# Kernel tuning notes

Hardware: AMD Instinct MI355X
Metric: run time of the kernel (lower is better)

The kernel has to match this reference:

```python
import jax, jax.numpy as jnp
import numpy as np

# irreps: node = 64x0e + 32x1o (dim 160), edge = 1x0e + 1x1o (dim 4)
N, E = 50000, 800000
MUL0, MUL1 = 64, 32
D = MUL0 + 3 * MUL1  # 160
INV3 = float(1.0 / np.sqrt(3.0))   # w3j(0,1,1) / w3j(1,1,0) component
INV6 = float(1.0 / np.sqrt(6.0))   # w3j(1,1,1) component (eps/sqrt(6))
C0 = float(1.0 / np.sqrt(MUL0 + MUL1))          # sqrt(dim_out=1 / fan_in=96) for 0e output
C1 = float(np.sqrt(3.0 / (MUL0 + 2 * MUL1)))    # sqrt(dim_out=3 / fan_in=128) for 1o output
LIN_S = float(1.0 / np.sqrt(MUL0))
LIN_V = float(1.0 / np.sqrt(MUL1))


def setup_inputs() -> dict:
    key = jax.random.key(0)
    ks = jax.random.split(key, 10)
    x = jax.random.normal(ks[0], (N, D), dtype=jnp.float32)
    sh = jax.random.normal(ks[1], (E, 4), dtype=jnp.float32)
    edge_index = jax.random.randint(ks[2], (2, E), 0, N, dtype=jnp.int64)
    # FullyConnectedTensorProduct path weights (mul2 = 1 squeezed out)
    W1 = jax.random.normal(ks[3], (MUL0, MUL0), dtype=jnp.float32)  # 0e x 0e -> 0e
    W2 = jax.random.normal(ks[4], (MUL1, MUL0), dtype=jnp.float32)  # 1o x 1o -> 0e
    W3 = jax.random.normal(ks[5], (MUL0, MUL1), dtype=jnp.float32)  # 0e x 1o -> 1o
    W4 = jax.random.normal(ks[6], (MUL1, MUL1), dtype=jnp.float32)  # 1o x 0e -> 1o
    W5 = jax.random.normal(ks[7], (MUL1, MUL1), dtype=jnp.float32)  # 1o x 1o -> 1o
    # equivariant Linear (block-diagonal per irrep type)
    Ws = jax.random.normal(ks[8], (MUL0, MUL0), dtype=jnp.float32)
    Wv = jax.random.normal(ks[9], (MUL1, MUL1), dtype=jnp.float32)
    return {"x": x, "sh": sh, "W1": W1, "W2": W2, "W3": W3, "W4": W4,
            "W5": W5, "Ws": Ws, "Wv": Wv, "edge_index": edge_index}


def reference(x, sh, W1, W2, W3, W4, W5, Ws, Wv, edge_index):
    n = x.shape[0]
    src, dst = edge_index[0], edge_index[1]
    s = x[:, :MUL0]                              # (N, 64)   0e
    v = x[:, MUL0:].reshape(n, MUL1, 3)          # (N, 32, 3) 1o
    ss, vv = s[src], v[src]                      # gather: (E,64), (E,32,3)
    e0 = sh[:, 0:1]                              # (E,1)
    e1 = sh[:, 1:4]                              # (E,3)

    # --- CG tensor product per edge ---
    # 0e output
    dot = jnp.einsum('eui,ei->eu', vv, e1)       # 1o x 1o -> 0e
    out0 = C0 * ((ss * e0) @ W1 + (dot * INV3) @ W2)          # (E,64)
    # 1o output
    p3 = (ss @ W3)[:, :, None] * e1[:, None, :] * INV3         # 0e x 1o -> 1o
    p4 = jnp.einsum('eui,uw->ewi', vv * e0[:, :, None], W4) * INV3  # 1o x 0e -> 1o
    p5 = jnp.einsum('eui,uw->ewi', jnp.cross(vv, e1[:, None, :]), W5) * INV6  # 1o x 1o -> 1o
    out1 = C1 * (p3 + p4 + p5)                   # (E,32,3)

    m = jnp.concatenate([out0, out1.reshape(-1, 3 * MUL1)], axis=1)  # (E,160)
    m_agg = jax.ops.segment_sum(m, dst, num_segments=n)              # scatter-add

    # --- equivariant Linear (block per irrep) ---
    hs = (m_agg[:, :MUL0] @ Ws) * LIN_S
    hv = jnp.einsum('nui,uw->nwi', m_agg[:, MUL0:].reshape(n, MUL1, 3), Wv) * LIN_V
    h = jnp.concatenate([hs, hv.reshape(n, 3 * MUL1)], axis=1)
    return x + jax.nn.relu(h)
```

## Files before the change

### kernel.cpp

```cpp
#include <hip/hip_runtime.h>

#define DFEAT 160

typedef float  f4v __attribute__((ext_vector_type(4)));
typedef short  s8v __attribute__((ext_vector_type(8)));

__device__ __constant__ float kINV3 = 0.57735026918962576451f;
__device__ __constant__ float kINV6 = 0.40824829046386301637f;
__device__ __constant__ float kC0   = 0.10206207261596575f;
__device__ __constant__ float kC1   = 0.15309310892394863f;
__device__ __constant__ float kLS   = 0.125f;
__device__ __constant__ float kLV   = 0.17677669529663687f;

#define WAVE_SYNC() do { \
    asm volatile("s_waitcnt lgkmcnt(0)" ::: "memory"); \
    __builtin_amdgcn_sched_barrier(0); \
} while (0)

#define MFMA(a, b, c) __builtin_amdgcn_mfma_f32_16x16x32_bf16((a), (b), (c), 0, 0, 0)

__device__ __forceinline__ unsigned f2bf(float f) {
    const unsigned u = __builtin_bit_cast(unsigned, f);
    const unsigned r = 0x7fffu + ((u >> 16) & 1u);
    return (u + r) >> 16;
}
__device__ __forceinline__ float bf2f(unsigned short u) {
    return __builtin_bit_cast(float, ((unsigned)u) << 16);
}

__global__ void hist_kernel(const int* __restrict__ dst, int* __restrict__ deg, int E) {
    for (int e = blockIdx.x * blockDim.x + threadIdx.x; e < E; e += gridDim.x * blockDim.x)
        atomicAdd(&deg[dst[e]], 1);
}

__global__ __launch_bounds__(256) void blocksum_kernel(const int* __restrict__ deg,
                                                       int* __restrict__ bsum, int N) {
    __shared__ int red[256];
    const int b = blockIdx.x, t = threadIdx.x;
    const int base = b * 1024;
    int s = 0;
    for (int i = t; i < 1024; i += 256) {
        const int idx = base + i;
        if (idx < N) s += (deg[idx] + 3) & ~3;
    }
    red[t] = s;
    __syncthreads();
    for (int off = 128; off > 0; off >>= 1) {
        if (t < off) red[t] += red[t + off];
        __syncthreads();
    }
    if (t == 0) bsum[b] = red[0];
}

__global__ void scanb_kernel(int* __restrict__ bsum, int nb, int* __restrict__ rowptrN) {
    if (threadIdx.x == 0 && blockIdx.x == 0) {
        int run = 0;
        for (int i = 0; i < nb; ++i) { const int v = bsum[i]; bsum[i] = run; run += v; }
        *rowptrN = run;
    }
}

__global__ __launch_bounds__(256) void scanfinal_kernel(const int* __restrict__ deg,
                                                        const int* __restrict__ bsum,
                                                        int* __restrict__ rowptr,
                                                        int* __restrict__ cursor,
                                                        int* __restrict__ src_sorted,
                                                        float4* __restrict__ sh_sorted,
                                                        int N) {
    __shared__ int ts[256];
    const int b = blockIdx.x, t = threadIdx.x;
    const int i0 = b * 1024 + t * 4;
    int dO[4], dP[4];
    #pragma unroll
    for (int j = 0; j < 4; ++j) {
        dO[j] = (i0 + j < N) ? deg[i0 + j] : 0;
        dP[j] = (dO[j] + 3) & ~3;
    }
    ts[t] = dP[0] + dP[1] + dP[2] + dP[3];
    __syncthreads();
    for (int off = 1; off < 256; off <<= 1) {
        const int v = (t >= off) ? ts[t - off] : 0;
        __syncthreads();
        ts[t] += v;
        __syncthreads();
    }
    int ex = bsum[b] + ((t == 0) ? 0 : ts[t - 1]);
    const float4 z4 = make_float4(0.f, 0.f, 0.f, 0.f);
    #pragma unroll
    for (int j = 0; j < 4; ++j) {
        if (i0 + j < N) {
            rowptr[i0 + j] = ex;
            cursor[i0 + j] = ex;
            for (int f = ex + dO[j]; f < ex + dP[j]; ++f) {
                src_sorted[f] = 0;
                sh_sorted[f] = z4;
            }
            ex += dP[j];
        }
    }
}

__global__ void scatter_kernel(const int* __restrict__ src, const int* __restrict__ dst,
                               const float4* __restrict__ sh, int* __restrict__ cursor,
                               int* __restrict__ src_sorted, float4* __restrict__ sh_sorted,
                               int E) {
    for (int e = blockIdx.x * blockDim.x + threadIdx.x; e < E; e += gridDim.x * blockDim.x) {
        const int pos = atomicAdd(&cursor[dst[e]], 1);
        src_sorted[pos] = src[e];
        sh_sorted[pos] = sh[e];
    }
}

__global__ __launch_bounds__(256) void prep_kernel(
    const float* __restrict__ x, int N,
    const float* __restrict__ W1, const float* __restrict__ W2,
    const float* __restrict__ W3, const float* __restrict__ W4,
    const float* __restrict__ W5, const float* __restrict__ Ws,
    const float* __restrict__ Wv,
    unsigned short* __restrict__ wtB, unsigned short* __restrict__ xq)
{
    const int total = 160 * 480 + N * 20;
    for (int i = blockIdx.x * 256 + threadIdx.x; i < total; i += gridDim.x * 256) {
        if (i < 160 * 480) {
            const int o = i;
            const int f = o / 480, k = o % 480;
            float v = 0.f;
            if (f < 64) {
                if (k < 64) {
                    float a = 0.f;
                    for (int m = 0; m < 64; ++m) a += W1[k * 64 + m] * Ws[m * 64 + f];
                    v = kLS * kC0 * a;
                } else if (k >= 256 && k < 288) {
                    float a = 0.f;
                    for (int m = 0; m < 64; ++m) a += W2[(k - 256) * 64 + m] * Ws[m * 64 + f];
                    v = kLS * kC0 * a;
                }
            } else {
                const int w = (f - 64) / 3, ii = (f - 64) % 3;
                if (k >= 64 + 64 * ii && k < 128 + 64 * ii) {
                    float a = 0.f;
                    const int kk = k - 64 - 64 * ii;
                    for (int m = 0; m < 32; ++m) a += W3[kk * 32 + m] * Wv[m * 32 + w];
                    v = kLV * kC1 * a;
                } else if (k >= 288 + 32 * ii && k < 320 + 32 * ii) {
                    float a = 0.f;
                    const int kk = k - 288 - 32 * ii;
                    for (int m = 0; m < 32; ++m) a += W4[kk * 32 + m] * Wv[m * 32 + w];
                    v = kLV * kC1 * a;
                } else if (k >= 384 + 32 * ii && k < 416 + 32 * ii) {
                    float a = 0.f;
                    const int kk = k - 384 - 32 * ii;
                    for (int m = 0; m < 32; ++m) a += W5[kk * 32 + m] * Wv[m * 32 + w];
                    v = kLV * kC1 * a;
                }
            }
            wtB[o] = (unsigned short)f2bf(v);
        } else {
            const int s = i - 160 * 480;
            const float4 a = ((const float4*)x)[2 * s + 0];
            const float4 b = ((const float4*)x)[2 * s + 1];
            int4 o;
            o.x = (int)(f2bf(a.x) | (f2bf(a.y) << 16));
            o.y = (int)(f2bf(a.z) | (f2bf(a.w) << 16));
            o.z = (int)(f2bf(b.x) | (f2bf(b.y) << 16));
            o.w = (int)(f2bf(b.z) | (f2bf(b.w) << 16));
            ((int4*)xq)[s] = o;
        }
    }
}

__global__ __launch_bounds__(256, 8) void agg_bf16_kernel(
    const unsigned short* __restrict__ xq, const float4* __restrict__ shs,
    const int* __restrict__ srcs, const int* __restrict__ rowptr,
    unsigned short* __restrict__ st_all, int N)
{
    const int tid  = threadIdx.x;
    const int lane = tid & 63;
    const int wid  = tid >> 6;
    const bool lo  = (lane < 32);
    const int  w   = lane & 31;

    for (int n = blockIdx.x * 4 + wid; n < N; n += gridDim.x * 4) {
        const int beg = rowptr[n];
        const int end = rowptr[n + 1];

        float r0 = 0.f, r1 = 0.f, r2 = 0.f, r3 = 0.f;
        float a2 = 0.f, a4x = 0.f, a4y = 0.f, a4z = 0.f;
        float a5x = 0.f, a5y = 0.f, a5z = 0.f;

#define PAIR(SA, SB, SHA, SHB) do { \
            const unsigned short* xa = xq + (size_t)(SA) * DFEAT; \
            const unsigned short* xb = xq + (size_t)(SB) * DFEAT; \
            const float xsA = bf2f(xa[lane]); \
            const float xsB = bf2f(xb[lane]); \
            const unsigned short* xh = lo ? xa : xb; \
            const float va = bf2f(xh[64 + 3 * w]); \
            const float vb = bf2f(xh[65 + 3 * w]); \
            const float vc = bf2f(xh[66 + 3 * w]); \
            r0 += (SHA).x * xsA;  r0 += (SHB).x * xsB; \
            r1 += (SHA).y * xsA;  r1 += (SHB).y * xsB; \
            r2 += (SHA).z * xsA;  r2 += (SHB).z * xsB; \
            r3 += (SHA).w * xsA;  r3 += (SHB).w * xsB; \
            const float he0  = lo ? (SHA).x : (SHB).x; \
            const float he1x = lo ? (SHA).y : (SHB).y; \
            const float he1y = lo ? (SHA).z : (SHB).z; \
            const float he1z = lo ? (SHA).w : (SHB).w; \
            a2  += va * he1x + vb * he1y + vc * he1z; \
            a4x += he0 * va;  a4y += he0 * vb;  a4z += he0 * vc; \
            a5x += vb * he1z;  a5x -= vc * he1y; \
            a5y += vc * he1x;  a5y -= va * he1z; \
            a5z += va * he1y;  a5z -= vb * he1x; \
        } while (0)

        for (int idx = beg; idx < end; idx += 4) {
            const int4 s4 = *(const int4*)(srcs + idx);
            const float4 shA = shs[idx + 0];
            const float4 shB = shs[idx + 1];
            const float4 shC = shs[idx + 2];
            const float4 shD = shs[idx + 3];
            PAIR(s4.x, s4.y, shA, shB);
            PAIR(s4.z, s4.w, shC, shD);
        }
#undef PAIR

        a2  += __shfl_xor(a2, 32);
        a4x += __shfl_xor(a4x, 32);
        a4y += __shfl_xor(a4y, 32);
        a4z += __shfl_xor(a4z, 32);
        a5x += __shfl_xor(a5x, 32);
        a5y += __shfl_xor(a5y, 32);
        a5z += __shfl_xor(a5z, 32);

        unsigned short* sr = st_all + (size_t)n * 480;
        sr[lane]       = (unsigned short)f2bf(r0);
        sr[64 + lane]  = (unsigned short)f2bf(kINV3 * r1);
        sr[128 + lane] = (unsigned short)f2bf(kINV3 * r2);
        sr[192 + lane] = (unsigned short)f2bf(kINV3 * r3);
        sr[256 + lane] = (unsigned short)f2bf(kINV3 * (lo ? a2 : a4x));
        sr[320 + lane] = (unsigned short)f2bf(lo ? (kINV3 * a4y) : (kINV3 * a4z));
        sr[384 + lane] = (unsigned short)f2bf(lo ? (kINV6 * a5x) : (kINV6 * a5y));
        if (lo) sr[448 + lane] = (unsigned short)f2bf(kINV6 * a5z);
    }
}

__global__ __launch_bounds__(256, 8) void agg_f32_kernel(
    const float* __restrict__ x, const float4* __restrict__ shs,
    const int* __restrict__ srcs, const int* __restrict__ rowptr,
    unsigned short* __restrict__ st_all, int N)
{
    const int tid  = threadIdx.x;
    const int lane = tid & 63;
    const int wid  = tid >> 6;
    const bool lo  = (lane < 32);
    const int  w   = lane & 31;

    for (int n = blockIdx.x * 4 + wid; n < N; n += gridDim.x * 4) {
        const int beg = rowptr[n];
        const int end = rowptr[n + 1];

        float r0 = 0.f, r1 = 0.f, r2 = 0.f, r3 = 0.f;
        float a2 = 0.f, a4x = 0.f, a4y = 0.f, a4z = 0.f;
        float a5x = 0.f, a5y = 0.f, a5z = 0.f;

#define PAIR(SA, SB, SHA, SHB) do { \
            const float* xa = x + (size_t)(SA) * DFEAT; \
            const float* xb = x + (size_t)(SB) * DFEAT; \
            const float xsA = xa[lane]; \
            const float xsB = xb[lane]; \
            const float* xh = lo ? xa : xb; \
            const float va = xh[64 + 3 * w]; \
            const float vb = xh[65 + 3 * w]; \
            const float vc = xh[66 + 3 * w]; \
            r0 += (SHA).x * xsA;  r0 += (SHB).x * xsB; \
            r1 += (SHA).y * xsA;  r1 += (SHB).y * xsB; \
            r2 += (SHA).z * xsA;  r2 += (SHB).z * xsB; \
            r3 += (SHA).w * xsA;  r3 += (SHB).w * xsB; \
            const float he0  = lo ? (SHA).x : (SHB).x; \
            const float he1x = lo ? (SHA).y : (SHB).y; \
            const float he1y = lo ? (SHA).z : (SHB).z; \
            const float he1z = lo ? (SHA).w : (SHB).w; \
            a2  += va * he1x + vb * he1y + vc * he1z; \
            a4x += he0 * va;  a4y += he0 * vb;  a4z += he0 * vc; \
            a5x += vb * he1z;  a5x -= vc * he1y; \
            a5y += vc * he1x;  a5y -= va * he1z; \
            a5z += va * he1y;  a5z -= vb * he1x; \
        } while (0)

        for (int idx = beg; idx < end; idx += 4) {
            const int4 s4 = *(const int4*)(srcs + idx);
            const float4 shA = shs[idx + 0];
            const float4 shB = shs[idx + 1];
            const float4 shC = shs[idx + 2];
            const float4 shD = shs[idx + 3];
            PAIR(s4.x, s4.y, shA, shB);
            PAIR(s4.z, s4.w, shC, shD);
        }
#undef PAIR

        a2  += __shfl_xor(a2, 32);
        a4x += __shfl_xor(a4x, 32);
        a4y += __shfl_xor(a4y, 32);
        a4z += __shfl_xor(a4z, 32);
        a5x += __shfl_xor(a5x, 32);
        a5y += __shfl_xor(a5y, 32);
        a5z += __shfl_xor(a5z, 32);

        unsigned short* sr = st_all + (size_t)n * 480;
        sr[lane]       = (unsigned short)f2bf(r0);
        sr[64 + lane]  = (unsigned short)f2bf(kINV3 * r1);
        sr[128 + lane] = (unsigned short)f2bf(kINV3 * r2);
        sr[192 + lane] = (unsigned short)f2bf(kINV3 * r3);
        sr[256 + lane] = (unsigned short)f2bf(kINV3 * (lo ? a2 : a4x));
        sr[320 + lane] = (unsigned short)f2bf(lo ? (kINV3 * a4y) : (kINV3 * a4z));
        sr[384 + lane] = (unsigned short)f2bf(lo ? (kINV6 * a5x) : (kINV6 * a5y));
        if (lo) sr[448 + lane] = (unsigned short)f2bf(kINV6 * a5z);
    }
}

__global__ __launch_bounds__(256, 4) void transform_kernel(
    const float* __restrict__ x, const unsigned short* __restrict__ st_all,
    const unsigned short* __restrict__ wtB, float* __restrict__ out, int N)
{
    __shared__ float sEp[4][16][17];
    const int tid  = threadIdx.x;
    const int lane = tid & 63;
    const int wid  = tid >> 6;
    const int l15  = lane & 15;
    const int pp   = lane >> 4;
    const int ntiles = (N + 15) >> 4;

    for (int tile = blockIdx.x * 4 + wid; tile < ntiles; tile += gridDim.x * 4) {
        const int n0 = tile * 16;
        const int nd = n0 + l15;
        const int ndc = (nd < N) ? nd : (N - 1);

        s8v a[15];
        #pragma unroll
        for (int kc = 0; kc < 15; ++kc)
            a[kc] = *(const s8v*)(st_all + (size_t)ndc * 480 + kc * 32 + pp * 8);

        for (int t = 0; t < 10; ++t) {
            f4v acc = (f4v){0.f, 0.f, 0.f, 0.f};
            const unsigned short* wrow = wtB + (size_t)(16 * t + l15) * 480 + pp * 8;
            if (t < 4) {
                acc = MFMA(a[0], *(const s8v*)(wrow + 0 * 32), acc);
                acc = MFMA(a[1], *(const s8v*)(wrow + 1 * 32), acc);
                acc = MFMA(a[8], *(const s8v*)(wrow + 8 * 32), acc);
            } else {
                #pragma unroll
                for (int kc = 2; kc <= 7; ++kc)
                    acc = MFMA(a[kc], *(const s8v*)(wrow + kc * 32), acc);
                #pragma unroll
                for (int kc = 9; kc <= 14; ++kc)
                    acc = MFMA(a[kc], *(const s8v*)(wrow + kc * 32), acc);
            }
            WAVE_SYNC();
            #pragma unroll
            for (int j = 0; j < 4; ++j)
                sEp[wid][pp * 4 + j][l15] = acc[j];
            WAVE_SYNC();
            #pragma unroll
            for (int it = 0; it < 4; ++it) {
                const int q  = it * 4 + pp;
                const int nq = n0 + q;
                if (nq < N) {
                    const float h = sEp[wid][q][l15];
                    const size_t off = (size_t)nq * DFEAT + 16 * t + l15;
                    out[off] = x[off] + fmaxf(h, 0.f);
                }
            }
        }
    }
}

extern "C" void kernel_launch(void* const* d_in, const int* in_sizes, int n_in,
                              void* d_out, int out_size, void* d_ws, size_t ws_size,
                              hipStream_t stream) {
    const float* x  = (const float*)d_in[0];
    const float* sh = (const float*)d_in[1];
    const float* W1 = (const float*)d_in[2];
    const float* W2 = (const float*)d_in[3];
    const float* W3 = (const float*)d_in[4];
    const float* W4 = (const float*)d_in[5];
    const float* W5 = (const float*)d_in[6];
    const float* Ws = (const float*)d_in[7];
    const float* Wv = (const float*)d_in[8];
    const int*   ei = (const int*)d_in[9];

    const int E = in_sizes[9] / 2;
    const int N = in_sizes[0] / DFEAT;
    const int* src = ei;
    const int* dst = ei + E;
    const int nb = (N + 1023) / 1024;
    const size_t Ep = (size_t)E + 3 * (size_t)N + 16;

    char* p = (char*)d_ws;
    float4* sh_sorted = (float4*)p;                 p += Ep * 16;
    unsigned short* st_all = (unsigned short*)p;    p += (size_t)N * 480 * 2;
    unsigned short* wtB = (unsigned short*)p;       p += 160 * 480 * 2;
    int* src_sorted = (int*)p;                      p += Ep * 4;
    int* deg = (int*)p;                             p += (size_t)N * 4;
    int* cursor = (int*)p;                          p += (size_t)N * 4;
    int* rowptr = (int*)p;                          p += ((size_t)N + 1) * 4;
    int* bsum = (int*)p;                            p += 1024;
    p = (char*)(((size_t)p + 15) & ~(size_t)15);
    unsigned short* xq = (unsigned short*)p;
    const size_t need_bf16 = (size_t)(p - (char*)d_ws) + (size_t)N * DFEAT * 2;
    const bool use_bf16 = (ws_size >= need_bf16);

    (void)hipMemsetAsync(deg, 0, (size_t)N * sizeof(int), stream);

    hist_kernel<<<1024, 256, 0, stream>>>(dst, deg, E);
    blocksum_kernel<<<nb, 256, 0, stream>>>(deg, bsum, N);
    scanb_kernel<<<1, 64, 0, stream>>>(bsum, nb, rowptr + N);
    scanfinal_kernel<<<nb, 256, 0, stream>>>(deg, bsum, rowptr, cursor,
                                             src_sorted, sh_sorted, N);
    scatter_kernel<<<1024, 256, 0, stream>>>(src, dst, (const float4*)sh, cursor,
                                             src_sorted, sh_sorted, E);
    if (use_bf16) {
        prep_kernel<<<2048, 256, 0, stream>>>(x, N, W1, W2, W3, W4, W5, Ws, Wv, wtB, xq);
        agg_bf16_kernel<<<2048, 256, 0, stream>>>(xq, (const float4*)sh_sorted,
                                                  src_sorted, rowptr, st_all, N);
    } else {
        prep_kernel<<<2048, 256, 0, stream>>>(x, 0, W1, W2, W3, W4, W5, Ws, Wv, wtB, xq);
        agg_f32_kernel<<<2048, 256, 0, stream>>>(x, (const float4*)sh_sorted,
                                                 src_sorted, rowptr, st_all, N);
    }
    transform_kernel<<<800, 256, 0, stream>>>(x, st_all, wtB, (float*)d_out, N);
}
```

Baseline: 234.3 us.

## Fuse edge aggregation with MFMA node transform through shared-memory staging

The bf16 aggregation kernel and the linear transform kernel are merged into one kernel. Each block handles a tile of 16 nodes: its four waves aggregate four nodes each into a padded LDS buffer, then run bf16 MFMAs against the precomputed weight matrix and write relu plus residual directly to the output. This removes the global round trip of the 480-wide per-node intermediate and one kernel launch. In exchange it adds block-wide barriers, gives each wave less independent gather work to hide latency, and launches one block per tile.

```diff
diff --git a/kernel.cpp b/kernel.cpp
--- a/kernel.cpp
+++ b/kernel.cpp
@@ -1,6 +1,7 @@
 #include <hip/hip_runtime.h>
 
 #define DFEAT 160
+#define STRIDE 488
 
 typedef float  f4v __attribute__((ext_vector_type(4)));
 typedef short  s8v __attribute__((ext_vector_type(8)));
@@ -169,77 +170,119 @@
     }
 }
 
-__global__ __launch_bounds__(256, 8) void agg_bf16_kernel(
-    const unsigned short* __restrict__ xq, const float4* __restrict__ shs,
-    const int* __restrict__ srcs, const int* __restrict__ rowptr,
-    unsigned short* __restrict__ st_all, int N)
+__global__ __launch_bounds__(256, 8) void fused_kernel(
+    const unsigned short* __restrict__ xq, const float* __restrict__ x,
+    const float4* __restrict__ shs, const int* __restrict__ srcs,
+    const int* __restrict__ rowptr, const unsigned short* __restrict__ wtB,
+    float* __restrict__ out, int N)
 {
+    __shared__ unsigned short st[16 * STRIDE];
+
     const int tid  = threadIdx.x;
     const int lane = tid & 63;
     const int wid  = tid >> 6;
     const bool lo  = (lane < 32);
     const int  w   = lane & 31;
-
-    for (int n = blockIdx.x * 4 + wid; n < N; n += gridDim.x * 4) {
-        const int beg = rowptr[n];
-        const int end = rowptr[n + 1];
-
-        float r0 = 0.f, r1 = 0.f, r2 = 0.f, r3 = 0.f;
-        float a2 = 0.f, a4x = 0.f, a4y = 0.f, a4z = 0.f;
-        float a5x = 0.f, a5y = 0.f, a5z = 0.f;
+    const int  l15 = lane & 15;
+    const int  pp  = lane >> 4;
+    const int ntiles = (N + 15) >> 4;
+
+    for (int tile = blockIdx.x; tile < ntiles; tile += gridDim.x) {
+        const int n0 = tile << 4;
+
+        for (int j = 0; j < 4; ++j) {
+            const int q = 4 * wid + j;
+            const int n = n0 + q;
+            if (n < N) {
+                const int beg = rowptr[n];
+                const int end = rowptr[n + 1];
+
+                float r0 = 0.f, r1 = 0.f, r2 = 0.f, r3 = 0.f;
+                float a2 = 0.f, a4x = 0.f, a4y = 0.f, a4z = 0.f;
+                float a5x = 0.f, a5y = 0.f, a5z = 0.f;
 
 #define PAIR(SA, SB, SHA, SHB) do { \
-            const unsigned short* xa = xq + (size_t)(SA) * DFEAT; \
-            const unsigned short* xb = xq + (size_t)(SB) * DFEAT; \
-            const float xsA = bf2f(xa[lane]); \
-            const float xsB = bf2f(xb[lane]); \
-            const unsigned short* xh = lo ? xa : xb; \
-            const float va = bf2f(xh[64 + 3 * w]); \
-            const float vb = bf2f(xh[65 + 3 * w]); \
-            const float vc = bf2f(xh[66 + 3 * w]); \
-            r0 += (SHA).x * xsA;  r0 += (SHB).x * xsB; \
-            r1 += (SHA).y * xsA;  r1 += (SHB).y * xsB; \
-            r2 += (SHA).z * xsA;  r2 += (SHB).z * xsB; \
-            r3 += (SHA).w * xsA;  r3 += (SHB).w * xsB; \
-            const float he0  = lo ? (SHA).x : (SHB).x; \
-            const float he1x = lo ? (SHA).y : (SHB).y; \
-            const float he1y = lo ? (SHA).z : (SHB).z; \
-            const float he1z = lo ? (SHA).w : (SHB).w; \
-            a2  += va * he1x + vb * he1y + vc * he1z; \
-            a4x += he0 * va;  a4y += he0 * vb;  a4z += he0 * vc; \
-            a5x += vb * he1z;  a5x -= vc * he1y; \
-            a5y += vc * he1x;  a5y -= va * he1z; \
-            a5z += va * he1y;  a5z -= vb * he1x; \
-        } while (0)
-
-        for (int idx = beg; idx < end; idx += 4) {
-            const int4 s4 = *(const int4*)(srcs + idx);
-            const float4 shA = shs[idx + 0];
-            const float4 shB = shs[idx + 1];
-            const float4 shC = shs[idx + 2];
-            const float4 shD = shs[idx + 3];
-            PAIR(s4.x, s4.y, shA, shB);
-            PAIR(s4.z, s4.w, shC, shD);
-        }
+                const unsigned short* xa = xq + (size_t)(SA) * DFEAT; \
+                const unsigned short* xb = xq + (size_t)(SB) * DFEAT; \
+                const float xsA = bf2f(xa[lane]); \
+                const float xsB = bf2f(xb[lane]); \
+                const unsigned short* xh = lo ? xa : xb; \
+                const float va = bf2f(xh[64 + 3 * w]); \
+                const float vb = bf2f(xh[65 + 3 * w]); \
+                const float vc = bf2f(xh[66 + 3 * w]); \
+                r0 += (SHA).x * xsA;  r0 += (SHB).x * xsB; \
+                r1 += (SHA).y * xsA;  r1 += (SHB).y * xsB; \
+                r2 += (SHA).z * xsA;  r2 += (SHB).z * xsB; \
+                r3 += (SHA).w * xsA;  r3 += (SHB).w * xsB; \
+                const float he0  = lo ? (SHA).x : (SHB).x; \
+                const float he1x = lo ? (SHA).y : (SHB).y; \
+                const float he1y = lo ? (SHA).z : (SHB).z; \
+                const float he1z = lo ? (SHA).w : (SHB).w; \
+                a2  += va * he1x + vb * he1y + vc * he1z; \
+                a4x += he0 * va;  a4y += he0 * vb;  a4z += he0 * vc; \
+                a5x += vb * he1z;  a5x -= vc * he1y; \
+                a5y += vc * he1x;  a5y -= va * he1z; \
+                a5z += va * he1y;  a5z -= vb * he1x; \
+            } while (0)
+
+                for (int idx = beg; idx < end; idx += 4) {
+                    const int4 s4 = *(const int4*)(srcs + idx);
+                    const float4 shA = shs[idx + 0];
+                    const float4 shB = shs[idx + 1];
+                    const float4 shC = shs[idx + 2];
+                    const float4 shD = shs[idx + 3];
+                    PAIR(s4.x, s4.y, shA, shB);
+                    PAIR(s4.z, s4.w, shC, shD);
+                }
 #undef PAIR
 
-        a2  += __shfl_xor(a2, 32);
-        a4x += __shfl_xor(a4x, 32);
-        a4y += __shfl_xor(a4y, 32);
-        a4z += __shfl_xor(a4z, 32);
-        a5x += __shfl_xor(a5x, 32);
-        a5y += __shfl_xor(a5y, 32);
-        a5z += __shfl_xor(a5z, 32);
-
-        unsigned short* sr = st_all + (size_t)n * 480;
-        sr[lane]       = (unsigned short)f2bf(r0);
-        sr[64 + lane]  = (unsigned short)f2bf(kINV3 * r1);
-        sr[128 + lane] = (unsigned short)f2bf(kINV3 * r2);
-        sr[192 + lane] = (unsigned short)f2bf(kINV3 * r3);
-        sr[256 + lane] = (unsigned short)f2bf(kINV3 * (lo ? a2 : a4x));
-        sr[320 + lane] = (unsigned short)f2bf(lo ? (kINV3 * a4y) : (kINV3 * a4z));
-        sr[384 + lane] = (unsigned short)f2bf(lo ? (kINV6 * a5x) : (kINV6 * a5y));
-        if (lo) sr[448 + lane] = (unsigned short)f2bf(kINV6 * a5z);
+                a2  += __shfl_xor(a2, 32);
+                a4x += __shfl_xor(a4x, 32);
+                a4y += __shfl_xor(a4y, 32);
+                a4z += __shfl_xor(a4z, 32);
+                a5x += __shfl_xor(a5x, 32);
+                a5y += __shfl_xor(a5y, 32);
+                a5z += __shfl_xor(a5z, 32);
+
+                unsigned short* sr = st + q * STRIDE;
+                sr[lane]       = (unsigned short)f2bf(r0);
+                sr[64 + lane]  = (unsigned short)f2bf(kINV3 * r1);
+                sr[128 + lane] = (unsigned short)f2bf(kINV3 * r2);
+                sr[192 + lane] = (unsigned short)f2bf(kINV3 * r3);
+                sr[256 + lane] = (unsigned short)f2bf(kINV3 * (lo ? a2 : a4x));
+                sr[320 + lane] = (unsigned short)f2bf(lo ? (kINV3 * a4y) : (kINV3 * a4z));
+                sr[384 + lane] = (unsigned short)f2bf(lo ? (kINV6 * a5x) : (kINV6 * a5y));
+                if (lo) sr[448 + lane] = (unsigned short)f2bf(kINV6 * a5z);
+            }
+        }
+        __syncthreads();
+
+        const unsigned short* arow = st + l15 * STRIDE + pp * 8;
+        for (int t = wid; t < 10; t += 4) {
+            f4v acc = (f4v){0.f, 0.f, 0.f, 0.f};
+            const unsigned short* wrow = wtB + (size_t)(16 * t + l15) * 480 + pp * 8;
+            if (t < 4) {
+                acc = MFMA(*(const s8v*)(arow + 0 * 32), *(const s8v*)(wrow + 0 * 32), acc);
+                acc = MFMA(*(const s8v*)(arow + 1 * 32), *(const s8v*)(wrow + 1 * 32), acc);
+                acc = MFMA(*(const s8v*)(arow + 8 * 32), *(const s8v*)(wrow + 8 * 32), acc);
+            } else {
+                #pragma unroll
+                for (int kc = 2; kc <= 7; ++kc)
+                    acc = MFMA(*(const s8v*)(arow + kc * 32), *(const s8v*)(wrow + kc * 32), acc);
+                #pragma unroll
+                for (int kc = 9; kc <= 14; ++kc)
+                    acc = MFMA(*(const s8v*)(arow + kc * 32), *(const s8v*)(wrow + kc * 32), acc);
+            }
+            #pragma unroll
+            for (int j = 0; j < 4; ++j) {
+                const int nq = n0 + pp * 4 + j;
+                if (nq < N) {
+                    const size_t off = (size_t)nq * DFEAT + 16 * t + l15;
+                    out[off] = x[off] + fmaxf(acc[j], 0.f);
+                }
+            }
+        }
+        __syncthreads();
     }
 }
 
@@ -392,6 +435,7 @@
     const int* src = ei;
     const int* dst = ei + E;
     const int nb = (N + 1023) / 1024;
+    const int ntiles = (N + 15) >> 4;
     const size_t Ep = (size_t)E + 3 * (size_t)N + 16;
 
     char* p = (char*)d_ws;
@@ -419,12 +463,13 @@
                                              src_sorted, sh_sorted, E);
     if (use_bf16) {
         prep_kernel<<<2048, 256, 0, stream>>>(x, N, W1, W2, W3, W4, W5, Ws, Wv, wtB, xq);
-        agg_bf16_kernel<<<2048, 256, 0, stream>>>(xq, (const float4*)sh_sorted,
-                                                  src_sorted, rowptr, st_all, N);
+        fused_kernel<<<ntiles, 256, 0, stream>>>(xq, x, (const float4*)sh_sorted,
+                                                 src_sorted, rowptr, wtB,
+                                                 (float*)d_out, N);
     } else {
         prep_kernel<<<2048, 256, 0, stream>>>(x, 0, W1, W2, W3, W4, W5, Ws, Wv, wtB, xq);
         agg_f32_kernel<<<2048, 256, 0, stream>>>(x, (const float4*)sh_sorted,
                                                  src_sorted, rowptr, st_all, N);
-    }
-    transform_kernel<<<800, 256, 0, stream>>>(x, st_all, wtB, (float*)d_out, N);
-}
+        transform_kernel<<<800, 256, 0, stream>>>(x, st_all, wtB, (float*)d_out, N);
+    }
+}
```

Result: no change. 233.6 us (-0.3%).
